# Optimization experiments

Hardware: AMD Instinct MI355X
Metric: run time of the kernel (lower is better)

## Reference

```python
import jax, jax.numpy as jnp
import numpy as np

NUM_CELLS = 91
NUM_MOVES = 4206
D = 64
NH = 4
HD = D // NH  # 16
FF = 2 * D   # 128
FILTERS = 128

# static hex grid indices (same as torch _hex_grid_indices)
_idx = [(r + 5, q + 5) for q in range(-5, 6) for r in range(-5, 6)
        if max(abs(q), abs(r), abs(q + r)) <= 5]
_HEX_ROWS = np.array([r for r, c in _idx], dtype=np.int32)
_HEX_COLS = np.array([c for r, c in _idx], dtype=np.int32)


def _ln(x, g, b, eps=1e-5):
    m = jnp.mean(x, axis=-1, keepdims=True)
    v = jnp.mean((x - m) ** 2, axis=-1, keepdims=True)
    return (x - m) * jax.lax.rsqrt(v + eps) * g + b


def setup_inputs() -> dict:
    key = jax.random.key(0)
    ks = jax.random.split(key, 24)
    B = 512
    s = lambda fan_in: 1.0 / np.sqrt(fan_in)
    return {
        "x": jax.random.normal(ks[0], (B, FILTERS, 11, 11), dtype=jnp.float32),
        "embed_w": jax.random.uniform(ks[1], (D, FILTERS), minval=-s(FILTERS), maxval=s(FILTERS)),
        "embed_b": jax.random.uniform(ks[2], (D,), minval=-s(FILTERS), maxval=s(FILTERS)),
        "pos": jax.random.normal(ks[3], (1, NUM_CELLS, D)) * 0.02,
        "in_w": jax.random.uniform(ks[4], (3 * D, D), minval=-s(D), maxval=s(D)),
        "in_b": jnp.zeros((3 * D,), jnp.float32),
        "out_w": jax.random.uniform(ks[5], (D, D), minval=-s(D), maxval=s(D)),
        "out_b": jnp.zeros((D,), jnp.float32),
        "ln1_g": jnp.ones((D,), jnp.float32),
        "ln1_b": jnp.zeros((D,), jnp.float32),
        "ln2_g": jnp.ones((D,), jnp.float32),
        "ln2_b": jnp.zeros((D,), jnp.float32),
        "ff1_w": jax.random.uniform(ks[6], (FF, D), minval=-s(D), maxval=s(D)),
        "ff1_b": jax.random.uniform(ks[7], (FF,), minval=-s(D), maxval=s(D)),
        "ff2_w": jax.random.uniform(ks[8], (D, FF), minval=-s(FF), maxval=s(FF)),
        "ff2_b": jax.random.uniform(ks[9], (D,), minval=-s(FF), maxval=s(FF)),
        "from_w": jax.random.uniform(ks[10], (D, D), minval=-s(D), maxval=s(D)),
        "from_b": jax.random.uniform(ks[11], (D,), minval=-s(D), maxval=s(D)),
        "to_w": jax.random.uniform(ks[12], (D, D), minval=-s(D), maxval=s(D)),
        "to_b": jax.random.uniform(ks[13], (D,), minval=-s(D), maxval=s(D)),
        "move_bias": jnp.zeros((NUM_MOVES,), jnp.float32),
        "move_from": jax.random.randint(ks[14], (NUM_MOVES,), 0, NUM_CELLS, dtype=jnp.int32),
        "move_to": jax.random.randint(ks[15], (NUM_MOVES,), 0, NUM_CELLS, dtype=jnp.int32),
    }


def reference(x, embed_w, embed_b, pos, in_w, in_b, out_w, out_b,
              ln1_g, ln1_b, ln2_g, ln2_b, ff1_w, ff1_b, ff2_w, ff2_b,
              from_w, from_b, to_w, to_b, move_bias, move_from, move_to):
    B = x.shape[0]
    # extract_hex: (B, C, 11, 11) -> (B, 91, C)
    feats = x[:, :, _HEX_ROWS, _HEX_COLS].transpose(0, 2, 1)
    h = feats @ embed_w.T + embed_b + pos  # (B, 91, D)

    # TransformerEncoderLayer, norm_first=True, eval (dropout=0), relu FFN
    hn = _ln(h, ln1_g, ln1_b)
    qkv = hn @ in_w.T + in_b  # (B, 91, 3D)
    q, k, v = jnp.split(qkv, 3, axis=-1)
    q = q.reshape(B, NUM_CELLS, NH, HD).transpose(0, 2, 1, 3)
    k = k.reshape(B, NUM_CELLS, NH, HD).transpose(0, 2, 1, 3)
    v = v.reshape(B, NUM_CELLS, NH, HD).transpose(0, 2, 1, 3)
    scores = jnp.einsum("bhqd,bhkd->bhqk", q, k) / np.sqrt(HD)
    attn = jax.nn.softmax(scores, axis=-1)
    o = jnp.einsum("bhqk,bhkd->bhqd", attn, v)
    o = o.transpose(0, 2, 1, 3).reshape(B, NUM_CELLS, D)
    h = h + (o @ out_w.T + out_b)
    hn = _ln(h, ln2_g, ln2_b)
    h = h + (jax.nn.relu(hn @ ff1_w.T + ff1_b) @ ff2_w.T + ff2_b)

    from_feats = h @ from_w.T + from_b  # (B, 91, D)
    to_feats = h @ to_w.T + to_b
    f = jnp.take(from_feats, move_from, axis=1)  # (B, 4206, D)
    t = jnp.take(to_feats, move_to, axis=1)      # (B, 4206, D)
    logits = jnp.sum(f * t, axis=-1) + move_bias  # (B, 4206)
    return logits
```

## Files before the change

### kernel.cpp

```cpp
#include <hip/hip_runtime.h>
#include <hip/hip_bf16.h>

typedef __attribute__((ext_vector_type(8))) short short8;
typedef __attribute__((ext_vector_type(4))) float f32x4;

#define NC    91
#define DM    64
#define CIN   128
#define NMOV  4206
#define MR    96
#define HP    68
#define QP    196
#define GP    96
#define NT    1024
#define NW    16

__constant__ int HEXOFF[NC] = {
  55,66,77,88,99,110,
  45,56,67,78,89,100,111,
  35,46,57,68,79,90,101,112,
  25,36,47,58,69,80,91,102,113,
  15,26,37,48,59,70,81,92,103,114,
  5,16,27,38,49,60,71,82,93,104,115,
  6,17,28,39,50,61,72,83,94,105,
  7,18,29,40,51,62,73,84,95,
  8,19,30,41,52,63,74,85,
  9,20,31,42,53,64,75,
  10,21,32,43,54,65
};

#define SWZ(row, col, PB) ((row)*(PB) + ((((((col)*2)>>4)) ^ ((row)&7)) << 4) + (((col)*2)&15))

__device__ __forceinline__ short f2bf(float f) {
  __hip_bfloat16 h = __float2bfloat16(f);
  return __builtin_bit_cast(short, h);
}

__device__ __forceinline__ short8 ldfrag128(const short* buf, int row, int k0) {
  return *(const short8*)((const char*)buf + SWZ(row, k0, 128));
}
__device__ __forceinline__ short8 ldfrag256(const short* buf, int row, int k0) {
  return *(const short8*)((const char*)buf + SWZ(row, k0, 256));
}
__device__ __forceinline__ void stb16_128(short* buf, int row, int col, float v) {
  *(short*)((char*)buf + SWZ(row, col, 128)) = f2bf(v);
}

__device__ __forceinline__ void stg8(short* buf, int row, int col, const float* src, int PB) {
  float4 f0 = *(const float4*)(src);
  float4 f1 = *(const float4*)(src + 4);
  short8 v;
  v[0]=f2bf(f0.x); v[1]=f2bf(f0.y); v[2]=f2bf(f0.z); v[3]=f2bf(f0.w);
  v[4]=f2bf(f1.x); v[5]=f2bf(f1.y); v[6]=f2bf(f1.z); v[7]=f2bf(f1.w);
  *(short8*)((char*)buf + (row)*(PB) + (((((col)*2)>>4) ^ ((row)&7)) << 4)) = v;
}

__device__ __forceinline__ void ln_group(const float* hbuf, short* ab16,
                                         const float* gw, const float* gb,
                                         int wid, int lane) {
  const int sub = lane >> 4;
  const int l16 = lane & 15;
  const float4 g4 = *(const float4*)&gw[l16*4];
  const float4 b4 = *(const float4*)&gb[l16*4];
  for (int g = wid; g < 23; g += NW) {
    int i = g*4 + sub;
    if (i < NC) {
      float4 v = *(const float4*)&hbuf[i*HP + l16*4];
      float s  = (v.x + v.y) + (v.z + v.w);
      float sq = fmaf(v.x,v.x, fmaf(v.y,v.y, fmaf(v.z,v.z, v.w*v.w)));
      #pragma unroll
      for (int off = 1; off < 16; off <<= 1) {
        s  += __shfl_xor(s, off, 64);
        sq += __shfl_xor(sq, off, 64);
      }
      float m  = s * (1.0f/64.0f);
      float vr = sq * (1.0f/64.0f) - m*m;
      float rs = rsqrtf(vr + 1e-5f);
      short4 o;
      o.x = f2bf((v.x - m)*rs*g4.x + b4.x);
      o.y = f2bf((v.y - m)*rs*g4.y + b4.y);
      o.z = f2bf((v.z - m)*rs*g4.z + b4.z);
      o.w = f2bf((v.w - m)*rs*g4.w + b4.w);
      *(short4*)((char*)ab16 + i*128 + (((l16>>1) ^ (i&7))<<4) + (l16&1)*8) = o;
    }
  }
}

__global__ __launch_bounds__(1024, 1)
void policy_fused(
    const float* __restrict__ x,
    const float* __restrict__ embed_w, const float* __restrict__ embed_b,
    const float* __restrict__ pos,
    const float* __restrict__ in_w,  const float* __restrict__ in_b,
    const float* __restrict__ out_w, const float* __restrict__ out_b,
    const float* __restrict__ ln1_g, const float* __restrict__ ln1_b,
    const float* __restrict__ ln2_g, const float* __restrict__ ln2_b,
    const float* __restrict__ ff1_w, const float* __restrict__ ff1_b,
    const float* __restrict__ ff2_w, const float* __restrict__ ff2_b,
    const float* __restrict__ from_w, const float* __restrict__ from_b,
    const float* __restrict__ to_w,  const float* __restrict__ to_b,
    const float* __restrict__ move_bias,
    const int* __restrict__ move_from, const int* __restrict__ move_to,
    float* __restrict__ out)
{
  __shared__ float hbuf[MR*HP];
  __shared__ float arena[18816];
  __shared__ short ab16[MR*64];
  __shared__ short wA[192*64];
  __shared__ short wB[64*128];

  const int tid  = threadIdx.x;
  const int lane = tid & 63;
  const int wid  = tid >> 6;
  const int l15  = lane & 15;
  const int kfr  = (lane >> 4) * 8;
  const int mfr  = (lane >> 4) * 4;
  const int b    = blockIdx.x;
  const float* xb = x + (size_t)b * (CIN*121);

  short* featsb = (short*)arena;
  for (int e = tid; e < 16*NC; e += NT) {
    int c0 = e / NC, i = e - c0*NC;
    float v[8];
    #pragma unroll
    for (int u = 0; u < 8; ++u) v[u] = xb[(c0*8 + u)*121 + HEXOFF[i]];
    short8 s8;
    #pragma unroll
    for (int u = 0; u < 8; ++u) s8[u] = f2bf(v[u]);
    *(short8*)((char*)featsb + i*256 + ((c0 ^ (i&7)) << 4)) = s8;
  }
  for (int e = tid; e < DM*CIN/8; e += NT) {
    int r = e >> 4, c8 = e & 15;
    stg8(wB, r, c8*8, &embed_w[r*CIN + c8*8], 256);
  }
  __syncthreads();

  for (int e = tid; e < 3*DM*DM/8; e += NT) {
    int r = e >> 3, c8 = e & 7;
    stg8(wA, r, c8*8, &in_w[r*DM + c8*8], 128);
  }
  for (int t = wid; t < 24; t += NW) {
    int mt = t >> 2, nt = t & 3;
    int ar = mt*16 + l15, br = nt*16 + l15;
    f32x4 acc = {0.f,0.f,0.f,0.f};
    #pragma unroll
    for (int kk = 0; kk < 4; ++kk) {
      short8 a = ldfrag256(featsb, ar, kk*32 + kfr);
      short8 w = ldfrag256(wB,      br, kk*32 + kfr);
      acc = __builtin_amdgcn_mfma_f32_16x16x32_bf16(a, w, acc, 0, 0, 0);
    }
    int col = nt*16 + l15;
    float eb = embed_b[col];
    #pragma unroll
    for (int i2 = 0; i2 < 4; ++i2) {
      int m = mt*16 + mfr + i2;
      float p = (m < NC) ? pos[m*DM + col] : 0.f;
      hbuf[m*HP + col] = acc[i2] + eb + p;
    }
  }
  __syncthreads();

  for (int e = tid; e < DM*DM/8; e += NT) {
    int r = e >> 3, c8 = e & 7;
    stg8((short*)wB, r, c8*8, &out_w[r*DM + c8*8], 128);
  }
  if (tid < 160) ((unsigned*)ab16)[2912 + tid] = 0;
  ln_group(hbuf, ab16, ln1_g, ln1_b, wid, lane);
  __syncthreads();

  float* qkv = arena;
  for (int t = wid; t < 72; t += NW) {
    int mt = t / 12, nt = t - mt*12;
    int ar = mt*16 + l15, br = nt*16 + l15;
    f32x4 acc = {0.f,0.f,0.f,0.f};
    #pragma unroll
    for (int kk = 0; kk < 2; ++kk) {
      short8 a = ldfrag128(ab16, ar, kk*32 + kfr);
      short8 w = ldfrag128(wA,   br, kk*32 + kfr);
      acc = __builtin_amdgcn_mfma_f32_16x16x32_bf16(a, w, acc, 0, 0, 0);
    }
    int col = nt*16 + l15;
    float bia = in_b[col];
    #pragma unroll
    for (int i2 = 0; i2 < 4; ++i2)
      qkv[(mt*16 + mfr + i2)*QP + col] = acc[i2] + bia;
  }
  __syncthreads();

  for (int e = tid; e < 2*DM*DM/8; e += NT) {
    int r = e >> 3, c8 = e & 7;
    stg8(wA, r, c8*8, &ff1_w[r*DM + c8*8], 128);
  }
  {
    const int q2   = tid >> 1;
    const int half = tid & 1;
    if (q2 < 4*NC) {
      const int h = q2 / NC;
      const int i = q2 - h*NC;
      const float CS = 0.25f * 1.4426950408889634f;
      const float* qr = &qkv[i*QP + h*16];
      float4 qa = *(const float4*)(qr+0),  qb = *(const float4*)(qr+4),
             qc = *(const float4*)(qr+8),  qd = *(const float4*)(qr+12);
      qa.x*=CS; qa.y*=CS; qa.z*=CS; qa.w*=CS;
      qb.x*=CS; qb.y*=CS; qb.z*=CS; qb.w*=CS;
      qc.x*=CS; qc.y*=CS; qc.z*=CS; qc.w*=CS;
      qd.x*=CS; qd.y*=CS; qd.z*=CS; qd.w*=CS;
      float4 oa = {0,0,0,0}, obv = {0,0,0,0}, ocv = {0,0,0,0}, odv = {0,0,0,0};
      float lrun = 0.0f;
      const int j0 = half ? 46 : 0;
      const int j1 = half ? NC : 46;
      for (int j = j0; j < j1; ++j) {
        const float* kr = &qkv[j*QP + DM + h*16];
        float4 ka = *(const float4*)(kr+0), kb = *(const float4*)(kr+4),
               kc = *(const float4*)(kr+8), kd = *(const float4*)(kr+12);
        float t0 = fmaf(qa.w,ka.w, fmaf(qa.z,ka.z, fmaf(qa.y,ka.y, qa.x*ka.x)));
        float t1 = fmaf(qb.w,kb.w, fmaf(qb.z,kb.z, fmaf(qb.y,kb.y, qb.x*kb.x)));
        float t2 = fmaf(qc.w,kc.w, fmaf(qc.z,kc.z, fmaf(qc.y,kc.y, qc.x*kc.x)));
        float t3 = fmaf(qd.w,kd.w, fmaf(qd.z,kd.z, fmaf(qd.y,kd.y, qd.x*kd.x)));
        float s2 = (t0+t1)+(t2+t3);
        float pw = exp2f(s2);
        lrun += pw;
        const float* vr = &qkv[j*QP + 2*DM + h*16];
        float4 va = *(const float4*)(vr+0), vb = *(const float4*)(vr+4),
               vc = *(const float4*)(vr+8), vd = *(const float4*)(vr+12);
        oa.x  = fmaf(pw, va.x, oa.x);  oa.y  = fmaf(pw, va.y, oa.y);
        oa.z  = fmaf(pw, va.z, oa.z);  oa.w  = fmaf(pw, va.w, oa.w);
        obv.x = fmaf(pw, vb.x, obv.x); obv.y = fmaf(pw, vb.y, obv.y);
        obv.z = fmaf(pw, vb.z, obv.z); obv.w = fmaf(pw, vb.w, obv.w);
        ocv.x = fmaf(pw, vc.x, ocv.x); ocv.y = fmaf(pw, vc.y, ocv.y);
        ocv.z = fmaf(pw, vc.z, ocv.z); ocv.w = fmaf(pw, vc.w, ocv.w);
        odv.x = fmaf(pw, vd.x, odv.x); odv.y = fmaf(pw, vd.y, odv.y);
        odv.z = fmaf(pw, vd.z, odv.z); odv.w = fmaf(pw, vd.w, odv.w);
      }
      lrun += __shfl_xor(lrun, 1, 64);
      #define MRG(c) c += __shfl_xor(c, 1, 64)
      MRG(oa.x); MRG(oa.y); MRG(oa.z); MRG(oa.w);
      MRG(obv.x); MRG(obv.y); MRG(obv.z); MRG(obv.w);
      MRG(ocv.x); MRG(ocv.y); MRG(ocv.z); MRG(ocv.w);
      MRG(odv.x); MRG(odv.y); MRG(odv.z); MRG(odv.w);
      #undef MRG
      float inv = 1.0f / lrun;
      float4 w0 = half ? ocv : oa;
      float4 w1 = half ? odv : obv;
      short8 ow;
      ow[0]=f2bf(w0.x*inv); ow[1]=f2bf(w0.y*inv); ow[2]=f2bf(w0.z*inv); ow[3]=f2bf(w0.w*inv);
      ow[4]=f2bf(w1.x*inv); ow[5]=f2bf(w1.y*inv); ow[6]=f2bf(w1.z*inv); ow[7]=f2bf(w1.w*inv);
      *(short8*)((char*)ab16 + SWZ(i, h*16 + half*8, 128)) = ow;
    }
  }
  __syncthreads();

  for (int t = wid; t < 24; t += NW) {
    int mt = t >> 2, nt = t & 3;
    int ar = mt*16 + l15, br = nt*16 + l15;
    f32x4 acc = {0.f,0.f,0.f,0.f};
    #pragma unroll
    for (int kk = 0; kk < 2; ++kk) {
      short8 a = ldfrag128(ab16,       ar, kk*32 + kfr);
      short8 w = ldfrag128((short*)wB, br, kk*32 + kfr);
      acc = __builtin_amdgcn_mfma_f32_16x16x32_bf16(a, w, acc, 0, 0, 0);
    }
    int col = nt*16 + l15;
    float ob = out_b[col];
    #pragma unroll
    for (int i2 = 0; i2 < 4; ++i2) {
      int m = mt*16 + mfr + i2;
      hbuf[m*HP + col] += acc[i2] + ob;
    }
  }
  __syncthreads();

  for (int e = tid; e < DM*CIN/8; e += NT) {
    int r = e >> 4, c8 = e & 15;
    stg8(wB, r, c8*8, &ff2_w[r*CIN + c8*8], 256);
  }
  ln_group(hbuf, ab16, ln2_g, ln2_b, wid, lane);
  __syncthreads();

  short* f1 = (short*)arena;
  for (int t = wid; t < 48; t += NW) {
    int mt = t >> 3, nt = t & 7;
    int ar = mt*16 + l15, br = nt*16 + l15;
    f32x4 acc = {0.f,0.f,0.f,0.f};
    #pragma unroll
    for (int kk = 0; kk < 2; ++kk) {
      short8 a = ldfrag128(ab16, ar, kk*32 + kfr);
      short8 w = ldfrag128(wA,   br, kk*32 + kfr);
      acc = __builtin_amdgcn_mfma_f32_16x16x32_bf16(a, w, acc, 0, 0, 0);
    }
    int col = nt*16 + l15;
    float bia = ff1_b[col];
    #pragma unroll
    for (int i2 = 0; i2 < 4; ++i2) {
      int m = mt*16 + mfr + i2;
      *(short*)((char*)f1 + SWZ(m, col, 256)) = f2bf(fmaxf(acc[i2] + bia, 0.f));
    }
  }
  __syncthreads();

  for (int e = tid; e < 2*DM*DM/8; e += NT) {
    int r = e >> 3, c8 = e & 7;
    const float* src = (r < DM) ? &from_w[r*DM + c8*8] : &to_w[(r-DM)*DM + c8*8];
    stg8(wA, r, c8*8, src, 128);
  }
  for (int t = wid; t < 24; t += NW) {
    int mt = t >> 2, nt = t & 3;
    int ar = mt*16 + l15, br = nt*16 + l15;
    f32x4 acc = {0.f,0.f,0.f,0.f};
    #pragma unroll
    for (int kk = 0; kk < 4; ++kk) {
      short8 a = ldfrag256(f1, ar, kk*32 + kfr);
      short8 w = ldfrag256(wB, br, kk*32 + kfr);
      acc = __builtin_amdgcn_mfma_f32_16x16x32_bf16(a, w, acc, 0, 0, 0);
    }
    int col = nt*16 + l15;
    float bia = ff2_b[col];
    #pragma unroll
    for (int i2 = 0; i2 < 4; ++i2) {
      int m = mt*16 + mfr + i2;
      stb16_128(ab16, m, col, hbuf[m*HP + col] + acc[i2] + bia);
    }
  }
  __syncthreads();

  short* Fb = (short*)arena;
  short* Tb = (short*)arena + 6144;
  for (int t = wid; t < 48; t += NW) {
    int mt = t >> 3, nt = t & 7;
    int ar = mt*16 + l15, br = nt*16 + l15;
    f32x4 acc = {0.f,0.f,0.f,0.f};
    #pragma unroll
    for (int kk = 0; kk < 2; ++kk) {
      short8 a = ldfrag128(ab16, ar, kk*32 + kfr);
      short8 w = ldfrag128(wA,   br, kk*32 + kfr);
      acc = __builtin_amdgcn_mfma_f32_16x16x32_bf16(a, w, acc, 0, 0, 0);
    }
    int col = nt*16 + l15;
    if (nt < 4) {
      float bia = from_b[col];
      #pragma unroll
      for (int i2 = 0; i2 < 4; ++i2)
        stb16_128(Fb, mt*16 + mfr + i2, col, acc[i2] + bia);
    } else {
      int c2 = col - 64;
      float bia = to_b[c2];
      #pragma unroll
      for (int i2 = 0; i2 < 4; ++i2)
        stb16_128(Tb, mt*16 + mfr + i2, c2, acc[i2] + bia);
    }
  }
  __syncthreads();

  float* G = arena + 6144;
  for (int t = wid; t < 36; t += NW) {
    int mt = t / 6, nt = t - mt*6;
    int ar = mt*16 + l15, br = nt*16 + l15;
    f32x4 acc = {0.f,0.f,0.f,0.f};
    #pragma unroll
    for (int kk = 0; kk < 2; ++kk) {
      short8 a = ldfrag128(Fb, ar, kk*32 + kfr);
      short8 w = ldfrag128(Tb, br, kk*32 + kfr);
      acc = __builtin_amdgcn_mfma_f32_16x16x32_bf16(a, w, acc, 0, 0, 0);
    }
    int col = nt*16 + l15;
    #pragma unroll
    for (int i2 = 0; i2 < 4; ++i2)
      G[(mt*16 + mfr + i2)*GP + col] = acc[i2];
  }
  __syncthreads();

  {
    float* ob = out + (size_t)b * NMOV;
    for (int m = tid; m < NMOV; m += NT) {
      ob[m] = G[move_from[m]*GP + move_to[m]] + move_bias[m];
    }
  }
}

extern "C" void kernel_launch(void* const* d_in, const int* in_sizes, int n_in,
                              void* d_out, int out_size, void* d_ws, size_t ws_size,
                              hipStream_t stream) {
  const float* x        = (const float*)d_in[0];
  const float* embed_w  = (const float*)d_in[1];
  const float* embed_b  = (const float*)d_in[2];
  const float* pos      = (const float*)d_in[3];
  const float* in_w     = (const float*)d_in[4];
  const float* in_b     = (const float*)d_in[5];
  const float* out_w    = (const float*)d_in[6];
  const float* out_b    = (const float*)d_in[7];
  const float* ln1_g    = (const float*)d_in[8];
  const float* ln1_b    = (const float*)d_in[9];
  const float* ln2_g    = (const float*)d_in[10];
  const float* ln2_b    = (const float*)d_in[11];
  const float* ff1_w    = (const float*)d_in[12];
  const float* ff1_b    = (const float*)d_in[13];
  const float* ff2_w    = (const float*)d_in[14];
  const float* ff2_b    = (const float*)d_in[15];
  const float* from_w   = (const float*)d_in[16];
  const float* from_b   = (const float*)d_in[17];
  const float* to_w     = (const float*)d_in[18];
  const float* to_b     = (const float*)d_in[19];
  const float* move_bias= (const float*)d_in[20];
  const int*   move_from= (const int*)d_in[21];
  const int*   move_to  = (const int*)d_in[22];

  int B = in_sizes[0] / (CIN * 121);
  policy_fused<<<dim3(B), dim3(NT), 0, stream>>>(
      x, embed_w, embed_b, pos, in_w, in_b, out_w, out_b,
      ln1_g, ln1_b, ln2_g, ln2_b, ff1_w, ff1_b, ff2_w, ff2_b,
      from_w, from_b, to_w, to_b, move_bias, move_from, move_to,
      (float*)d_out);
}
```

Baseline: 58.09 us.

## Pre-convert weights to bf16 in workspace, read MFMA fragments from global, shrink LDS

Adds a small pre-kernel that converts all projection weights to bf16 once per call into the workspace. The fused kernel then loads weight MFMA fragments directly from global/L2 instead of staging each weight matrix in LDS per block. Q/K/V are also stored as bf16 in head-major layout, which shrinks shared memory, and launch bounds are relaxed so more blocks can be resident per CU. In exchange, every block issues unswizzled global weight loads inside the MFMA loops, there is an extra kernel launch, and Q/K/V lose precision.

Result: slower. 86.83 us (+49.5%).

```diff
diff --git a/kernel.cpp b/kernel.cpp
--- a/kernel.cpp
+++ b/kernel.cpp
@@ -10,10 +10,17 @@
 #define NMOV  4206
 #define MR    96
 #define HP    68
-#define QP    196
-#define GP    96
+#define GP    92
 #define NT    1024
 #define NW    16
+
+#define W_EMBED 0
+#define W_IN    8192
+#define W_OUT   20480
+#define W_FF1   24576
+#define W_FF2   32768
+#define W_FT    40960
+#define W_TOTAL 49152
 
 __constant__ int HEXOFF[NC] = {
   55,66,77,88,99,110,
@@ -35,6 +42,8 @@
   __hip_bfloat16 h = __float2bfloat16(f);
   return __builtin_bit_cast(short, h);
 }
+__device__ __forceinline__ float bflo(unsigned u){ return __builtin_bit_cast(float, u << 16); }
+__device__ __forceinline__ float bfhi(unsigned u){ return __builtin_bit_cast(float, u & 0xffff0000u); }
 
 __device__ __forceinline__ short8 ldfrag128(const short* buf, int row, int k0) {
   return *(const short8*)((const char*)buf + SWZ(row, k0, 128));
@@ -45,14 +54,8 @@
 __device__ __forceinline__ void stb16_128(short* buf, int row, int col, float v) {
   *(short*)((char*)buf + SWZ(row, col, 128)) = f2bf(v);
 }
-
-__device__ __forceinline__ void stg8(short* buf, int row, int col, const float* src, int PB) {
-  float4 f0 = *(const float4*)(src);
-  float4 f1 = *(const float4*)(src + 4);
-  short8 v;
-  v[0]=f2bf(f0.x); v[1]=f2bf(f0.y); v[2]=f2bf(f0.z); v[3]=f2bf(f0.w);
-  v[4]=f2bf(f1.x); v[5]=f2bf(f1.y); v[6]=f2bf(f1.z); v[7]=f2bf(f1.w);
-  *(short8*)((char*)buf + (row)*(PB) + (((((col)*2)>>4) ^ ((row)&7)) << 4)) = v;
+__device__ __forceinline__ short8 gfrag(const short* gw, int row, int K, int k0) {
+  return *(const short8*)(gw + row*K + k0);
 }
 
 __device__ __forceinline__ void ln_group(const float* hbuf, short* ab16,
@@ -86,28 +89,42 @@
   }
 }
 
-__global__ __launch_bounds__(1024, 1)
+__global__ __launch_bounds__(256)
+void prep_w(const float* __restrict__ embed_w, const float* __restrict__ in_w,
+            const float* __restrict__ out_w, const float* __restrict__ ff1_w,
+            const float* __restrict__ ff2_w, const float* __restrict__ from_w,
+            const float* __restrict__ to_w, short* __restrict__ ws)
+{
+  int i = blockIdx.x*256 + threadIdx.x;
+  if (i >= W_TOTAL) return;
+  float v;
+  if      (i < 8192)  v = embed_w[i];
+  else if (i < 20480) v = in_w[i - 8192];
+  else if (i < 24576) v = out_w[i - 20480];
+  else if (i < 32768) v = ff1_w[i - 24576];
+  else if (i < 40960) v = ff2_w[i - 32768];
+  else if (i < 45056) v = from_w[i - 40960];
+  else                v = to_w[i - 45056];
+  ws[i] = f2bf(v);
+}
+
+__global__ __launch_bounds__(1024, 8)
 void policy_fused(
     const float* __restrict__ x,
-    const float* __restrict__ embed_w, const float* __restrict__ embed_b,
-    const float* __restrict__ pos,
-    const float* __restrict__ in_w,  const float* __restrict__ in_b,
-    const float* __restrict__ out_w, const float* __restrict__ out_b,
+    const float* __restrict__ embed_b, const float* __restrict__ pos,
+    const float* __restrict__ in_b,  const float* __restrict__ out_b,
     const float* __restrict__ ln1_g, const float* __restrict__ ln1_b,
     const float* __restrict__ ln2_g, const float* __restrict__ ln2_b,
-    const float* __restrict__ ff1_w, const float* __restrict__ ff1_b,
-    const float* __restrict__ ff2_w, const float* __restrict__ ff2_b,
-    const float* __restrict__ from_w, const float* __restrict__ from_b,
-    const float* __restrict__ to_w,  const float* __restrict__ to_b,
+    const float* __restrict__ ff1_b, const float* __restrict__ ff2_b,
+    const float* __restrict__ from_b, const float* __restrict__ to_b,
     const float* __restrict__ move_bias,
     const int* __restrict__ move_from, const int* __restrict__ move_to,
+    const short* __restrict__ ws,
     float* __restrict__ out)
 {
-  __shared__ float hbuf[MR*HP];
-  __shared__ float arena[18816];
+  __shared__ float Abuf[8736];
+  __shared__ float Bbuf[MR*HP];
   __shared__ short ab16[MR*64];
-  __shared__ short wA[192*64];
-  __shared__ short wB[64*128];
 
   const int tid  = threadIdx.x;
   const int lane = tid & 63;
@@ -118,7 +135,14 @@
   const int b    = blockIdx.x;
   const float* xb = x + (size_t)b * (CIN*121);
 
-  short* featsb = (short*)arena;
+  float* hbuf   = Bbuf;
+  short* featsb = (short*)Abuf;
+  short* qb = (short*)Abuf;
+  short* kb = qb + 4*NC*16;
+  short* vb = kb + 4*NC*16;
+  short* f1 = (short*)Abuf;
+  float* G  = Abuf;
+
   for (int e = tid; e < 16*NC; e += NT) {
     int c0 = e / NC, i = e - c0*NC;
     float v[8];
@@ -129,16 +153,9 @@
     for (int u = 0; u < 8; ++u) s8[u] = f2bf(v[u]);
     *(short8*)((char*)featsb + i*256 + ((c0 ^ (i&7)) << 4)) = s8;
   }
-  for (int e = tid; e < DM*CIN/8; e += NT) {
-    int r = e >> 4, c8 = e & 15;
-    stg8(wB, r, c8*8, &embed_w[r*CIN + c8*8], 256);
-  }
-  __syncthreads();
-
-  for (int e = tid; e < 3*DM*DM/8; e += NT) {
-    int r = e >> 3, c8 = e & 7;
-    stg8(wA, r, c8*8, &in_w[r*DM + c8*8], 128);
-  }
+  if (tid < 320) ((unsigned*)featsb)[5824 + tid] = 0;
+  __syncthreads();
+
   for (int t = wid; t < 24; t += NW) {
     int mt = t >> 2, nt = t & 3;
     int ar = mt*16 + l15, br = nt*16 + l15;
@@ -146,7 +163,7 @@
     #pragma unroll
     for (int kk = 0; kk < 4; ++kk) {
       short8 a = ldfrag256(featsb, ar, kk*32 + kfr);
-      short8 w = ldfrag256(wB,      br, kk*32 + kfr);
+      short8 w = gfrag(ws + W_EMBED, br, 128, kk*32 + kfr);
       acc = __builtin_amdgcn_mfma_f32_16x16x32_bf16(a, w, acc, 0, 0, 0);
     }
     int col = nt*16 + l15;
@@ -160,15 +177,10 @@
   }
   __syncthreads();
 
-  for (int e = tid; e < DM*DM/8; e += NT) {
-    int r = e >> 3, c8 = e & 7;
-    stg8((short*)wB, r, c8*8, &out_w[r*DM + c8*8], 128);
-  }
   if (tid < 160) ((unsigned*)ab16)[2912 + tid] = 0;
   ln_group(hbuf, ab16, ln1_g, ln1_b, wid, lane);
   __syncthreads();
 
-  float* qkv = arena;
   for (int t = wid; t < 72; t += NW) {
     int mt = t / 12, nt = t - mt*12;
     int ar = mt*16 + l15, br = nt*16 + l15;
@@ -176,21 +188,22 @@
     #pragma unroll
     for (int kk = 0; kk < 2; ++kk) {
       short8 a = ldfrag128(ab16, ar, kk*32 + kfr);
-      short8 w = ldfrag128(wA,   br, kk*32 + kfr);
+      short8 w = gfrag(ws + W_IN, br, 64, kk*32 + kfr);
       acc = __builtin_amdgcn_mfma_f32_16x16x32_bf16(a, w, acc, 0, 0, 0);
     }
     int col = nt*16 + l15;
     float bia = in_b[col];
-    #pragma unroll
-    for (int i2 = 0; i2 < 4; ++i2)
-      qkv[(mt*16 + mfr + i2)*QP + col] = acc[i2] + bia;
-  }
-  __syncthreads();
-
-  for (int e = tid; e < 2*DM*DM/8; e += NT) {
-    int r = e >> 3, c8 = e & 7;
-    stg8(wA, r, c8*8, &ff1_w[r*DM + c8*8], 128);
-  }
+    int hl = (col & 63) >> 4;
+    int d  = col & 15;
+    short* dst = (col < 64) ? qb : ((col < 128) ? kb : vb);
+    #pragma unroll
+    for (int i2 = 0; i2 < 4; ++i2) {
+      int m = mt*16 + mfr + i2;
+      if (m < NC) dst[(hl*NC + m)*16 + d] = f2bf(acc[i2] + bia);
+    }
+  }
+  __syncthreads();
+
   {
     const int q2   = tid >> 1;
     const int half = tid & 1;
@@ -198,39 +211,41 @@
       const int h = q2 / NC;
       const int i = q2 - h*NC;
       const float CS = 0.25f * 1.4426950408889634f;
-      const float* qr = &qkv[i*QP + h*16];
-      float4 qa = *(const float4*)(qr+0),  qb = *(const float4*)(qr+4),
-             qc = *(const float4*)(qr+8),  qd = *(const float4*)(qr+12);
-      qa.x*=CS; qa.y*=CS; qa.z*=CS; qa.w*=CS;
-      qb.x*=CS; qb.y*=CS; qb.z*=CS; qb.w*=CS;
-      qc.x*=CS; qc.y*=CS; qc.z*=CS; qc.w*=CS;
-      qd.x*=CS; qd.y*=CS; qd.z*=CS; qd.w*=CS;
+      const unsigned* qp = (const unsigned*)(qb + (h*NC + i)*16);
+      uint4 qv0 = *(const uint4*)qp, qv1 = *(const uint4*)(qp + 4);
+      float q0=bflo(qv0.x)*CS, q1=bfhi(qv0.x)*CS, q2f=bflo(qv0.y)*CS, q3=bfhi(qv0.y)*CS,
+            q4=bflo(qv0.z)*CS, q5=bfhi(qv0.z)*CS, q6=bflo(qv0.w)*CS, q7=bfhi(qv0.w)*CS,
+            q8=bflo(qv1.x)*CS, q9=bfhi(qv1.x)*CS, qA=bflo(qv1.y)*CS, qB=bfhi(qv1.y)*CS,
+            qC=bflo(qv1.z)*CS, qD=bfhi(qv1.z)*CS, qE=bflo(qv1.w)*CS, qF=bfhi(qv1.w)*CS;
+      const unsigned* kp = (const unsigned*)(kb + h*NC*16);
+      const unsigned* vp = (const unsigned*)(vb + h*NC*16);
       float4 oa = {0,0,0,0}, obv = {0,0,0,0}, ocv = {0,0,0,0}, odv = {0,0,0,0};
       float lrun = 0.0f;
       const int j0 = half ? 46 : 0;
       const int j1 = half ? NC : 46;
       for (int j = j0; j < j1; ++j) {
-        const float* kr = &qkv[j*QP + DM + h*16];
-        float4 ka = *(const float4*)(kr+0), kb = *(const float4*)(kr+4),
-               kc = *(const float4*)(kr+8), kd = *(const float4*)(kr+12);
-        float t0 = fmaf(qa.w,ka.w, fmaf(qa.z,ka.z, fmaf(qa.y,ka.y, qa.x*ka.x)));
-        float t1 = fmaf(qb.w,kb.w, fmaf(qb.z,kb.z, fmaf(qb.y,kb.y, qb.x*kb.x)));
-        float t2 = fmaf(qc.w,kc.w, fmaf(qc.z,kc.z, fmaf(qc.y,kc.y, qc.x*kc.x)));
-        float t3 = fmaf(qd.w,kd.w, fmaf(qd.z,kd.z, fmaf(qd.y,kd.y, qd.x*kd.x)));
-        float s2 = (t0+t1)+(t2+t3);
-        float pw = exp2f(s2);
+        uint4 k0v = *(const uint4*)(kp + j*8);
+        uint4 k1v = *(const uint4*)(kp + j*8 + 4);
+        float t0 = fmaf(q1, bfhi(k0v.x), q0*bflo(k0v.x));
+        t0 = fmaf(q3, bfhi(k0v.y), fmaf(q2f, bflo(k0v.y), t0));
+        float t1 = fmaf(q5, bfhi(k0v.z), q4*bflo(k0v.z));
+        t1 = fmaf(q7, bfhi(k0v.w), fmaf(q6, bflo(k0v.w), t1));
+        float t2 = fmaf(q9, bfhi(k1v.x), q8*bflo(k1v.x));
+        t2 = fmaf(qB, bfhi(k1v.y), fmaf(qA, bflo(k1v.y), t2));
+        float t3 = fmaf(qD, bfhi(k1v.z), qC*bflo(k1v.z));
+        t3 = fmaf(qF, bfhi(k1v.w), fmaf(qE, bflo(k1v.w), t3));
+        float pw = exp2f((t0+t1)+(t2+t3));
         lrun += pw;
-        const float* vr = &qkv[j*QP + 2*DM + h*16];
-        float4 va = *(const float4*)(vr+0), vb = *(const float4*)(vr+4),
-               vc = *(const float4*)(vr+8), vd = *(const float4*)(vr+12);
-        oa.x  = fmaf(pw, va.x, oa.x);  oa.y  = fmaf(pw, va.y, oa.y);
-        oa.z  = fmaf(pw, va.z, oa.z);  oa.w  = fmaf(pw, va.w, oa.w);
-        obv.x = fmaf(pw, vb.x, obv.x); obv.y = fmaf(pw, vb.y, obv.y);
-        obv.z = fmaf(pw, vb.z, obv.z); obv.w = fmaf(pw, vb.w, obv.w);
-        ocv.x = fmaf(pw, vc.x, ocv.x); ocv.y = fmaf(pw, vc.y, ocv.y);
-        ocv.z = fmaf(pw, vc.z, ocv.z); ocv.w = fmaf(pw, vc.w, ocv.w);
-        odv.x = fmaf(pw, vd.x, odv.x); odv.y = fmaf(pw, vd.y, odv.y);
-        odv.z = fmaf(pw, vd.z, odv.z); odv.w = fmaf(pw, vd.w, odv.w);
+        uint4 v0v = *(const uint4*)(vp + j*8);
+        uint4 v1v = *(const uint4*)(vp + j*8 + 4);
+        oa.x  = fmaf(pw, bflo(v0v.x), oa.x);  oa.y  = fmaf(pw, bfhi(v0v.x), oa.y);
+        oa.z  = fmaf(pw, bflo(v0v.y), oa.z);  oa.w  = fmaf(pw, bfhi(v0v.y), oa.w);
+        obv.x = fmaf(pw, bflo(v0v.z), obv.x); obv.y = fmaf(pw, bfhi(v0v.z), obv.y);
+        obv.z = fmaf(pw, bflo(v0v.w), obv.z); obv.w = fmaf(pw, bfhi(v0v.w), obv.w);
+        ocv.x = fmaf(pw, bflo(v1v.x), ocv.x); ocv.y = fmaf(pw, bfhi(v1v.x), ocv.y);
+        ocv.z = fmaf(pw, bflo(v1v.y), ocv.z); ocv.w = fmaf(pw, bfhi(v1v.y), ocv.w);
+        odv.x = fmaf(pw, bflo(v1v.z), odv.x); odv.y = fmaf(pw, bfhi(v1v.z), odv.y);
+        odv.z = fmaf(pw, bflo(v1v.w), odv.z); odv.w = fmaf(pw, bfhi(v1v.w), odv.w);
       }
       lrun += __shfl_xor(lrun, 1, 64);
       #define MRG(c) c += __shfl_xor(c, 1, 64)
@@ -256,8 +271,8 @@
     f32x4 acc = {0.f,0.f,0.f,0.f};
     #pragma unroll
     for (int kk = 0; kk < 2; ++kk) {
-      short8 a = ldfrag128(ab16,       ar, kk*32 + kfr);
-      short8 w = ldfrag128((short*)wB, br, kk*32 + kfr);
+      short8 a = ldfrag128(ab16, ar, kk*32 + kfr);
+      short8 w = gfrag(ws + W_OUT, br, 64, kk*32 + kfr);
       acc = __builtin_amdgcn_mfma_f32_16x16x32_bf16(a, w, acc, 0, 0, 0);
     }
     int col = nt*16 + l15;
@@ -270,14 +285,9 @@
   }
   __syncthreads();
 
-  for (int e = tid; e < DM*CIN/8; e += NT) {
-    int r = e >> 4, c8 = e & 15;
-    stg8(wB, r, c8*8, &ff2_w[r*CIN + c8*8], 256);
-  }
   ln_group(hbuf, ab16, ln2_g, ln2_b, wid, lane);
   __syncthreads();
 
-  short* f1 = (short*)arena;
   for (int t = wid; t < 48; t += NW) {
     int mt = t >> 3, nt = t & 7;
     int ar = mt*16 + l15, br = nt*16 + l15;
@@ -285,7 +295,7 @@
     #pragma unroll
     for (int kk = 0; kk < 2; ++kk) {
       short8 a = ldfrag128(ab16, ar, kk*32 + kfr);
-      short8 w = ldfrag128(wA,   br, kk*32 + kfr);
+      short8 w = gfrag(ws + W_FF1, br, 64, kk*32 + kfr);
       acc = __builtin_amdgcn_mfma_f32_16x16x32_bf16(a, w, acc, 0, 0, 0);
     }
     int col = nt*16 + l15;
@@ -298,11 +308,6 @@
   }
   __syncthreads();
 
-  for (int e = tid; e < 2*DM*DM/8; e += NT) {
-    int r = e >> 3, c8 = e & 7;
-    const float* src = (r < DM) ? &from_w[r*DM + c8*8] : &to_w[(r-DM)*DM + c8*8];
-    stg8(wA, r, c8*8, src, 128);
-  }
   for (int t = wid; t < 24; t += NW) {
     int mt = t >> 2, nt = t & 3;
     int ar = mt*16 + l15, br = nt*16 + l15;
@@ -310,7 +315,7 @@
     #pragma unroll
     for (int kk = 0; kk < 4; ++kk) {
       short8 a = ldfrag256(f1, ar, kk*32 + kfr);
-      short8 w = ldfrag256(wB, br, kk*32 + kfr);
+      short8 w = gfrag(ws + W_FF2, br, 128, kk*32 + kfr);
       acc = __builtin_amdgcn_mfma_f32_16x16x32_bf16(a, w, acc, 0, 0, 0);
     }
     int col = nt*16 + l15;
@@ -323,8 +328,8 @@
   }
   __syncthreads();
 
-  short* Fb = (short*)arena;
-  short* Tb = (short*)arena + 6144;
+  short* Fb = (short*)Bbuf;
+  short* Tb = (short*)Bbuf + 6144;
   for (int t = wid; t < 48; t += NW) {
     int mt = t >> 3, nt = t & 7;
     int ar = mt*16 + l15, br = nt*16 + l15;
@@ -332,7 +337,7 @@
     #pragma unroll
     for (int kk = 0; kk < 2; ++kk) {
       short8 a = ldfrag128(ab16, ar, kk*32 + kfr);
-      short8 w = ldfrag128(wA,   br, kk*32 + kfr);
+      short8 w = gfrag(ws + W_FT, br, 64, kk*32 + kfr);
       acc = __builtin_amdgcn_mfma_f32_16x16x32_bf16(a, w, acc, 0, 0, 0);
     }
     int col = nt*16 + l15;
@@ -351,7 +356,6 @@
   }
   __syncthreads();
 
-  float* G = arena + 6144;
   for (int t = wid; t < 36; t += NW) {
     int mt = t / 6, nt = t - mt*6;
     int ar = mt*16 + l15, br = nt*16 + l15;
@@ -363,9 +367,13 @@
       acc = __builtin_amdgcn_mfma_f32_16x16x32_bf16(a, w, acc, 0, 0, 0);
     }
     int col = nt*16 + l15;
-    #pragma unroll
-    for (int i2 = 0; i2 < 4; ++i2)
-      G[(mt*16 + mfr + i2)*GP + col] = acc[i2];
+    if (col < GP) {
+      #pragma unroll
+      for (int i2 = 0; i2 < 4; ++i2) {
+        int m = mt*16 + mfr + i2;
+        if (m < NC) G[m*GP + col] = acc[i2];
+      }
+    }
   }
   __syncthreads();
 
@@ -404,10 +412,14 @@
   const int*   move_from= (const int*)d_in[21];
   const int*   move_to  = (const int*)d_in[22];
 
+  short* wsb = (short*)d_ws;
+  prep_w<<<dim3((W_TOTAL + 255)/256), dim3(256), 0, stream>>>(
+      embed_w, in_w, out_w, ff1_w, ff2_w, from_w, to_w, wsb);
+
   int B = in_sizes[0] / (CIN * 121);
   policy_fused<<<dim3(B), dim3(NT), 0, stream>>>(
-      x, embed_w, embed_b, pos, in_w, in_b, out_w, out_b,
-      ln1_g, ln1_b, ln2_g, ln2_b, ff1_w, ff1_b, ff2_w, ff2_b,
-      from_w, from_b, to_w, to_b, move_bias, move_from, move_to,
-      (float*)d_out);
-}
+      x, embed_b, pos, in_b, out_b,
+      ln1_g, ln1_b, ln2_g, ln2_b, ff1_b, ff2_b,
+      from_b, to_b, move_bias, move_from, move_to,
+      (const short*)wsb, (float*)d_out);
+}
```
